# Kernel tuning notes

Hardware: AMD Instinct MI355X
Metric: run time of the kernel (lower is better)

## Reference

```python
import jax, jax.numpy as jnp
import numpy as np

D_MODEL = 512
N_HEADS = 8
KV_OPTS = (8, 4, 1)
D_K = D_MODEL // N_HEADS


def setup_inputs() -> dict:
    key = jax.random.key(0)
    ks = jax.random.split(key, 32)
    it = iter(ks)
    s = 0.02
    inp = {"x": jax.random.normal(next(it), (64, 1024, D_MODEL), dtype=jnp.float32)}
    # router params
    inp["r_w1"] = jax.random.normal(next(it), (D_MODEL, D_MODEL // 4), jnp.float32) * s
    inp["r_b1"] = jnp.zeros((D_MODEL // 4,), jnp.float32)
    inp["r_w2"] = jax.random.normal(next(it), (D_MODEL // 4, len(KV_OPTS)), jnp.float32) * s
    inp["r_b2"] = jnp.zeros((len(KV_OPTS),), jnp.float32)
    # per-expert GQA params
    for i, nkv in enumerate(KV_OPTS):
        inp[f"wq{i}"] = jax.random.normal(next(it), (D_MODEL, D_MODEL), jnp.float32) * s
        inp[f"wk{i}"] = jax.random.normal(next(it), (D_MODEL, nkv * D_K), jnp.float32) * s
        inp[f"wv{i}"] = jax.random.normal(next(it), (D_MODEL, nkv * D_K), jnp.float32) * s
        inp[f"wo{i}"] = jax.random.normal(next(it), (D_MODEL, D_MODEL), jnp.float32) * s
    return inp


def gqa(x, wq, wk, wv, wo, n_kv):
    B, S, _ = x.shape
    groups = N_HEADS // n_kv
    q = (x @ wq).reshape(B, S, N_HEADS, D_K).transpose(0, 2, 1, 3)  # [B,H,S,Dk]
    k = (x @ wk).reshape(B, S, n_kv, D_K).transpose(0, 2, 1, 3)     # [B,Kv,S,Dk]
    v = (x @ wv).reshape(B, S, n_kv, D_K).transpose(0, 2, 1, 3)
    k = jnp.repeat(k, groups, axis=1)
    v = jnp.repeat(v, groups, axis=1)
    scores = jnp.einsum('bhqd,bhkd->bhqk', q, k) / jnp.sqrt(jnp.float32(D_K))
    attn = jax.nn.softmax(scores, axis=-1)
    out = jnp.einsum('bhqk,bhkd->bhqd', attn, v)
    out = out.transpose(0, 2, 1, 3).reshape(B, S, D_MODEL)
    return out @ wo


def reference(x, r_w1, r_b1, r_w2, r_b2,
              wq0, wk0, wv0, wo0,
              wq1, wk1, wv1, wo1,
              wq2, wk2, wv2, wo2):
    routing_input = x.mean(axis=1)                      # [B, D]
    logits = jax.nn.relu(routing_input @ r_w1 + r_b1) @ r_w2 + r_b2
    sel = jnp.argmax(jax.nn.softmax(logits, axis=-1), axis=-1)  # [B]

    params = [(wq0, wk0, wv0, wo0), (wq1, wk1, wv1, wo1), (wq2, wk2, wv2, wo2)]
    out = jnp.zeros_like(x)
    for i, nkv in enumerate(KV_OPTS):
        yi = gqa(x, *params[i], nkv)                    # [B,S,D]
        mask = (sel == i)[:, None, None]
        out = jnp.where(mask, yi, out)
    return out
```

## Files before the change

### kernel.cpp

```cpp
#include <hip/hip_runtime.h>
#include <hip/hip_bf16.h>

typedef __hip_bfloat16 bf16;
typedef __attribute__((ext_vector_type(8))) short short8;
typedef __attribute__((ext_vector_type(4))) float f32x4;
typedef __attribute__((ext_vector_type(16))) float f32x16;

#define MFMA_BF16(a,b,c) __builtin_amdgcn_mfma_f32_16x16x32_bf16(a,b,c,0,0,0)
#define MFMA32(a,b,c)    __builtin_amdgcn_mfma_f32_32x32x16_bf16(a,b,c,0,0,0)

#if __has_builtin(__builtin_amdgcn_exp2f)
#define EXPFN(x) __builtin_amdgcn_exp2f(x)
#define QSCALE 0.1803368801111204f
#else
#define EXPFN(x) __expf(x)
#define QSCALE 0.125f
#endif

__device__ __forceinline__ unsigned short bfbits(float f){
  bf16 h = __float2bfloat16(f);
  return __builtin_bit_cast(unsigned short, h);
}
__device__ __forceinline__ unsigned packbf(float a, float b){
  return (unsigned)bfbits(a) | ((unsigned)bfbits(b) << 16);
}

__device__ __forceinline__ void glds16(const void* g, void* l){
  __builtin_amdgcn_global_load_lds(
      (const __attribute__((address_space(1))) unsigned int*)(size_t)g,
      (__attribute__((address_space(3))) unsigned int*)l, 16, 0, 0);
}

__global__ __launch_bounds__(256) void xconv(const float* __restrict__ x, bf16* __restrict__ xb){
  size_t i = ((size_t)blockIdx.x*256 + threadIdx.x)*8;
  float4 a = *(const float4*)(x+i);
  float4 b = *(const float4*)(x+i+4);
  union { unsigned short u[8]; uint4 v; } p;
  p.u[0]=bfbits(a.x); p.u[1]=bfbits(a.y); p.u[2]=bfbits(a.z); p.u[3]=bfbits(a.w);
  p.u[4]=bfbits(b.x); p.u[5]=bfbits(b.y); p.u[6]=bfbits(b.z); p.u[7]=bfbits(b.w);
  *(uint4*)(xb+i) = p.v;
}

__global__ __launch_bounds__(256)
void wconv(const float* __restrict__ w0, const float* __restrict__ w1, const float* __restrict__ w2,
           int N0, int N1, int N2, bf16* o0, bf16* o1, bf16* o2){
  int e = blockIdx.z;
  const float* W = e==0?w0:(e==1?w1:w2);
  int N = e==0?N0:(e==1?N1:N2);
  bf16* out = e==0?o0:(e==1?o1:o2);
  int n0 = blockIdx.y*64; if (n0 >= N) return;
  int k0 = blockIdx.x*64;
  __shared__ float tile[64][65];
  int t = threadIdx.x;
#pragma unroll
  for (int j=0;j<16;++j){
    int ee = j*256+t; int r = ee>>6, c = ee&63;
    tile[r][c] = W[(size_t)(k0+r)*N + n0+c];
  }
  __syncthreads();
#pragma unroll
  for (int j=0;j<16;++j){
    int ee = j*256+t; int n = ee>>6, kk = ee&63;
    out[(size_t)(n0+n)*512 + k0+kk] = __float2bfloat16(tile[kk][n]);
  }
}

__global__ void mean_part_kernel(const float* __restrict__ x, float* __restrict__ part){
  int b = blockIdx.x, ch = blockIdx.y;
  const float* xb = x + ((size_t)b*1024 + (size_t)ch*64)*512;
  for (int dd = threadIdx.x; dd < 512; dd += 256){
    float a = 0.f;
    for (int s = 0; s < 64; ++s) a += xb[(size_t)s*512 + dd];
    part[((size_t)b*16 + ch)*512 + dd] = a;
  }
}

__global__ void mean_final_kernel(const float* __restrict__ part, float* __restrict__ ri){
  int b = blockIdx.x;
  for (int dd = threadIdx.x; dd < 512; dd += 256){
    float a = 0.f;
    for (int c = 0; c < 16; ++c) a += part[((size_t)b*16 + c)*512 + dd];
    ri[(size_t)b*512 + dd] = a * (1.f/1024.f);
  }
}

__global__ void router_kernel(const float* __restrict__ ri,
                              const float* __restrict__ w1, const float* __restrict__ b1,
                              const float* __restrict__ w2, const float* __restrict__ b2,
                              int* __restrict__ sel){
  int b = blockIdx.x, t = threadIdx.x;
  __shared__ float h[128];
  __shared__ float lg[3];
  const float* rib = ri + (size_t)b*512;
  float acc = b1[t];
  for (int d = 0; d < 512; ++d) acc += rib[d]*w1[(size_t)d*128 + t];
  h[t] = fmaxf(acc, 0.f);
  __syncthreads();
  if (t < 3){
    float a = b2[t];
    for (int j = 0; j < 128; ++j) a += h[j]*w2[j*3 + t];
    lg[t] = a;
  }
  __syncthreads();
  if (t == 0){
    int best = 0; float bv = lg[0];
    if (lg[1] > bv){ bv = lg[1]; best = 1; }
    if (lg[2] > bv){ bv = lg[2]; best = 2; }
    sel[b] = best;
  }
}

template<int OUTMODE>
__global__ __launch_bounds__(256)
void gemm_mfma(const bf16* __restrict__ A,
               const bf16* __restrict__ Wt0, const bf16* __restrict__ Wt1, const bf16* __restrict__ Wt2,
               int N0, int N1, int N2,
               const int* __restrict__ sel, float oscale,
               void* __restrict__ outp){
  int b = blockIdx.z;
  int se = sel[b];
  const bf16* W = se==0?Wt0:(se==1?Wt1:Wt2);
  int N = se==0?N0:(se==1?N1:N2);
  int nb = blockIdx.y*64;
  if (nb >= N) return;
  int mb = blockIdx.x*128;
  __shared__ __align__(16) bf16 As[128*64];
  __shared__ __align__(16) bf16 Bs[64*64];
  int t = threadIdx.x, lane = t&63, w = t>>6, gg = lane>>4, cl = lane&15;
  f32x4 acc[2][4] = {};
  const bf16* Ab = A + ((size_t)b*1024 + mb)*512;
  const bf16* Wb = W + (size_t)nb*512;

  for (int k0 = 0; k0 < 512; k0 += 64){
#pragma unroll
    for (int j=0;j<4;++j){
      int o = (j*256+t)*16;
      int r = o>>7;
      int gs = ((o>>4)&7) ^ (r&7);
      glds16(Ab + (size_t)r*512 + k0 + gs*8, (char*)As + o);
    }
#pragma unroll
    for (int j=0;j<2;++j){
      int o = (j*256+t)*16;
      int r = o>>7;
      int gs = ((o>>4)&7) ^ (r&7);
      glds16(Wb + (size_t)r*512 + k0 + gs*8, (char*)Bs + o);
    }
    __syncthreads();

    short8 af[2][2], bfr[4][2];
#pragma unroll
    for (int mf=0;mf<2;++mf)
#pragma unroll
      for (int ks=0;ks<2;++ks){
        int r = w*32 + mf*16 + cl;
        int off = (ks*64 + gg*16) ^ ((r&7)<<4);
        af[mf][ks] = *(const short8*)((const char*)As + r*128 + off);
      }
#pragma unroll
    for (int nf=0;nf<4;++nf)
#pragma unroll
      for (int ks=0;ks<2;++ks){
        int r = nf*16 + cl;
        int off = (ks*64 + gg*16) ^ ((r&7)<<4);
        bfr[nf][ks] = *(const short8*)((const char*)Bs + r*128 + off);
      }
#pragma unroll
    for (int mf=0;mf<2;++mf)
#pragma unroll
      for (int nf=0;nf<4;++nf)
#pragma unroll
        for (int ks=0;ks<2;++ks)
          acc[mf][nf] = MFMA_BF16(af[mf][ks], bfr[nf][ks], acc[mf][nf]);
    __syncthreads();
  }

#pragma unroll
  for (int mf=0;mf<2;++mf)
#pragma unroll
    for (int nf=0;nf<4;++nf){
      int row = mb + w*32 + mf*16 + gg*4;
      int col = nb + nf*16 + cl;
      if (OUTMODE==0){
        bf16* C = (bf16*)outp;
#pragma unroll
        for (int i=0;i<4;++i)
          C[((size_t)b*1024 + row+i)*512 + col] = __float2bfloat16(acc[mf][nf][i]*oscale);
      } else if (OUTMODE==1){
        union { unsigned short u[4]; uint2 v; } pk;
#pragma unroll
        for (int i=0;i<4;++i) pk.u[i] = bfbits(acc[mf][nf][i]);
        *(uint2*)((bf16*)outp + ((size_t)b*512 + col)*1024 + row) = pk.v;
      } else {
        float* C = (float*)outp;
#pragma unroll
        for (int i=0;i<4;++i)
          C[((size_t)b*1024 + row+i)*512 + col] = acc[mf][nf][i];
      }
    }
}

__global__ __launch_bounds__(256, 4)
void attn_mfma(const bf16* __restrict__ Q, const bf16* __restrict__ K,
               const bf16* __restrict__ Vt, const int* __restrict__ sel,
               bf16* __restrict__ AO){
  int b = blockIdx.z, h = blockIdx.y, q0 = blockIdx.x*128;
  int se = sel[b];
  int nkv = se==0?8:(se==1?4:1);
  int kvh = h/(8/nkv);
  __shared__ __align__(16) bf16 Ks[2][64*64];
  __shared__ __align__(16) bf16 Vs[2][64*64];
  int t = threadIdx.x, l = t&63, w = t>>6, cl = l&31, hi = l>>5;
  const bf16* Kb = K + (size_t)b*1024*512 + (size_t)kvh*64;
  const bf16* Vb = Vt + ((size_t)b*512 + (size_t)kvh*64)*1024;
  const bf16* Qg = Q + ((size_t)b*1024 + q0 + w*32 + cl)*512 + h*64;

  short8 qf0 = *(const short8*)(Qg + hi*8);
  short8 qf1 = *(const short8*)(Qg + 16 + hi*8);
  short8 qf2 = *(const short8*)(Qg + 32 + hi*8);
  short8 qf3 = *(const short8*)(Qg + 48 + hi*8);

  f32x16 accO0 = {}, accO1 = {};
  float lrow = 0.f;
  int swz = (cl&7)<<4;

#define STAGE(CUR, S0) { \
  _Pragma("unroll") for (int j=0;j<2;++j){ \
    int o = (j*256+t)*16; int r = o>>7; int gs = ((o>>4)&7)^(r&7); \
    glds16(Kb + (size_t)((S0)+r)*512 + gs*8, (char*)Ks[CUR] + o); \
    glds16(Vb + (size_t)r*1024 + (S0) + gs*8, (char*)Vs[CUR] + o); \
  } }

  STAGE(0, 0)
  __syncthreads();
  int cur = 0;
  for (int kt=0; kt<16; ++kt){
    if (kt<15) STAGE(cur^1, (kt+1)*64)

    const char* Kt_ = (const char*)Ks[cur];
    const char* Vt_ = (const char*)Vs[cur];

    f32x16 sc0 = {}, sc1 = {};
#pragma unroll
    for (int ks=0;ks<4;++ks){
      int off = (ks*32 + hi*16) ^ swz;
      short8 kf0 = *(const short8*)(Kt_ + (size_t)cl*128 + off);
      short8 kf1 = *(const short8*)(Kt_ + (size_t)(32+cl)*128 + off);
      short8 qq = ks==0?qf0:(ks==1?qf1:(ks==2?qf2:qf3));
      sc0 = MFMA32(kf0, qq, sc0);
      sc1 = MFMA32(kf1, qq, sc1);
    }

    float ts0=0.f, ts1=0.f, ts2=0.f, ts3=0.f;
#pragma unroll
    for (int r=0;r<16;r+=2){
      float a0 = EXPFN(sc0[r]);   float a1 = EXPFN(sc0[r+1]);
      float a2 = EXPFN(sc1[r]);   float a3 = EXPFN(sc1[r+1]);
      sc0[r]=a0; sc0[r+1]=a1; sc1[r]=a2; sc1[r+1]=a3;
      ts0+=a0; ts1+=a1; ts2+=a2; ts3+=a3;
    }
    lrow += (ts0+ts1)+(ts2+ts3);

    unsigned pA0[4],pB0[4],pA1[4],pB1[4];
#pragma unroll
    for (int m=0;m<4;++m){
      pA0[m]=packbf(sc0[4*m+0],sc0[4*m+1]); pB0[m]=packbf(sc0[4*m+2],sc0[4*m+3]);
      pA1[m]=packbf(sc1[4*m+0],sc1[4*m+1]); pB1[m]=packbf(sc1[4*m+2],sc1[4*m+3]);
    }
    unsigned oA0[4],oB0[4],oA1[4],oB1[4];
#pragma unroll
    for (int m=0;m<4;++m){
      oA0[m]=__shfl_xor(pA0[m],32); oB0[m]=__shfl_xor(pB0[m],32);
      oA1[m]=__shfl_xor(pA1[m],32); oB1[m]=__shfl_xor(pB1[m],32);
    }
    short8 pF[4];
#pragma unroll
    for (int f=0;f<2;++f){
      uint4 u;
      u.x = hi ? oA0[2*f+1] : pA0[2*f];
      u.y = hi ? oB0[2*f+1] : pB0[2*f];
      u.z = hi ? pA0[2*f+1] : oA0[2*f];
      u.w = hi ? pB0[2*f+1] : oB0[2*f];
      pF[f] = __builtin_bit_cast(short8, u);
      uint4 v;
      v.x = hi ? oA1[2*f+1] : pA1[2*f];
      v.y = hi ? oB1[2*f+1] : pB1[2*f];
      v.z = hi ? pA1[2*f+1] : oA1[2*f];
      v.w = hi ? pB1[2*f+1] : oB1[2*f];
      pF[2+f] = __builtin_bit_cast(short8, v);
    }

#pragma unroll
    for (int ks2=0;ks2<4;++ks2){
      int off = (ks2*32 + hi*16) ^ swz;
      short8 vf0 = *(const short8*)(Vt_ + (size_t)cl*128 + off);
      short8 vf1 = *(const short8*)(Vt_ + (size_t)(32+cl)*128 + off);
      accO0 = MFMA32(vf0, pF[ks2], accO0);
      accO1 = MFMA32(vf1, pF[ks2], accO1);
    }
    __syncthreads();
    cur ^= 1;
  }
#undef STAGE

  float lfull = lrow + __shfl_xor(lrow, 32);
  float inv = 1.f/lfull;
  int row = q0 + w*32 + cl;
  bf16* Ao = AO + ((size_t)b*1024 + row)*512 + h*64;
#pragma unroll
  for (int u=0;u<4;++u){
    union{ unsigned short s[4]; uint2 v; } P0, P1;
#pragma unroll
    for (int j2=0;j2<4;++j2){
      P0.s[j2] = bfbits(accO0[4*u+j2]*inv);
      P1.s[j2] = bfbits(accO1[4*u+j2]*inv);
    }
    *(uint2*)(Ao + 8*u + 4*hi) = P0.v;
    *(uint2*)(Ao + 32 + 8*u + 4*hi) = P1.v;
  }
}

extern "C" void kernel_launch(void* const* d_in, const int* in_sizes, int n_in,
                              void* d_out, int out_size, void* d_ws, size_t ws_size,
                              hipStream_t stream){
  const float* x    = (const float*)d_in[0];
  const float* r_w1 = (const float*)d_in[1];
  const float* r_b1 = (const float*)d_in[2];
  const float* r_w2 = (const float*)d_in[3];
  const float* r_b2 = (const float*)d_in[4];
  const float* wq[3] = {(const float*)d_in[5], (const float*)d_in[9],  (const float*)d_in[13]};
  const float* wk[3] = {(const float*)d_in[6], (const float*)d_in[10], (const float*)d_in[14]};
  const float* wv[3] = {(const float*)d_in[7], (const float*)d_in[11], (const float*)d_in[15]};
  const float* wo[3] = {(const float*)d_in[8], (const float*)d_in[12], (const float*)d_in[16]};

  char* ws = (char*)d_ws;
  int*   sel      = (int*)ws;
  float* ri       = (float*)(ws + 4096);
  float* partials = (float*)(ws + 4096 + 131072);
  bf16*  Wtbuf    = (bf16*)(ws + 4096 + 131072 + 2097152);
  const size_t NE = (size_t)64*1024*512;
  bf16* xb = (bf16*)(ws + ((size_t)4<<20));
  bf16* Qb = xb + NE;
  bf16* Kb = Qb + NE;
  bf16* Vt = Kb + NE;
  bf16* AO = xb;

  xconv<<<16384, 256, 0, stream>>>(x, xb);
  mean_part_kernel<<<dim3(64,16), 256, 0, stream>>>(x, partials);
  mean_final_kernel<<<64, 256, 0, stream>>>(partials, ri);
  router_kernel<<<64, 128, 0, stream>>>(ri, r_w1, r_b1, r_w2, r_b2, sel);

  {
    bf16 *o0 = Wtbuf, *o1 = o0 + (size_t)512*512, *o2 = o1 + (size_t)512*512;
    wconv<<<dim3(8,8,3), 256, 0, stream>>>(wq[0],wq[1],wq[2], 512,512,512, o0,o1,o2);
    gemm_mfma<0><<<dim3(8,8,64), 256, 0, stream>>>(xb, o0,o1,o2, 512,512,512, sel, (float)QSCALE, Qb);
  }
  {
    bf16 *o0 = Wtbuf, *o1 = o0 + (size_t)512*512, *o2 = o1 + (size_t)256*512;
    wconv<<<dim3(8,8,3), 256, 0, stream>>>(wk[0],wk[1],wk[2], 512,256,64, o0,o1,o2);
    gemm_mfma<0><<<dim3(8,8,64), 256, 0, stream>>>(xb, o0,o1,o2, 512,256,64, sel, 1.0f, Kb);
  }
  {
    bf16 *o0 = Wtbuf, *o1 = o0 + (size_t)512*512, *o2 = o1 + (size_t)256*512;
    wconv<<<dim3(8,8,3), 256, 0, stream>>>(wv[0],wv[1],wv[2], 512,256,64, o0,o1,o2);
    gemm_mfma<1><<<dim3(8,8,64), 256, 0, stream>>>(xb, o0,o1,o2, 512,256,64, sel, 1.0f, Vt);
  }

  attn_mfma<<<dim3(8,8,64), 256, 0, stream>>>(Qb, Kb, Vt, sel, AO);

  {
    bf16 *o0 = Wtbuf, *o1 = o0 + (size_t)512*512, *o2 = o1 + (size_t)512*512;
    wconv<<<dim3(8,8,3), 256, 0, stream>>>(wo[0],wo[1],wo[2], 512,512,512, o0,o1,o2);
    gemm_mfma<2><<<dim3(8,8,64), 256, 0, stream>>>(AO, o0,o1,o2, 512,512,512, sel, 1.0f, (float*)d_out);
  }
}
```

Before: 466.7 us.

## Fuse x conversion with mean partials, widen GEMM N tile, tweak attention scheduling

Merges the fp32-to-bf16 conversion of x with the per-chunk mean partial sums, so x is read once instead of twice. Templates the projection GEMM on its N tile width and uses 128-wide tiles for the Q and output projections, giving more A-tile reuse per block and fewer blocks. In attention, raises wave priority around the MFMA loops and halves the cross-lane shuffles when building the P fragments. The wider tile raises register and LDS use per block, and the fused conversion kernel runs fewer, longer blocks.

Measured after the change: 441.2 us. 5.5% less time.

```diff
diff --git a/kernel.cpp b/kernel.cpp
--- a/kernel.cpp
+++ b/kernel.cpp
@@ -31,14 +31,31 @@
       (__attribute__((address_space(3))) unsigned int*)l, 16, 0, 0);
 }
 
-__global__ __launch_bounds__(256) void xconv(const float* __restrict__ x, bf16* __restrict__ xb){
-  size_t i = ((size_t)blockIdx.x*256 + threadIdx.x)*8;
-  float4 a = *(const float4*)(x+i);
-  float4 b = *(const float4*)(x+i+4);
-  union { unsigned short u[8]; uint4 v; } p;
-  p.u[0]=bfbits(a.x); p.u[1]=bfbits(a.y); p.u[2]=bfbits(a.z); p.u[3]=bfbits(a.w);
-  p.u[4]=bfbits(b.x); p.u[5]=bfbits(b.y); p.u[6]=bfbits(b.z); p.u[7]=bfbits(b.w);
-  *(uint4*)(xb+i) = p.v;
+__global__ __launch_bounds__(256)
+void xconv_mean(const float* __restrict__ x, bf16* __restrict__ xb, float* __restrict__ part){
+  int b = blockIdx.x, ch = blockIdx.y, t = threadIdx.x;
+  size_t base = ((size_t)b*1024 + (size_t)ch*64)*512;
+  const float2* xp = (const float2*)(x + base);
+  unsigned* op = (unsigned*)(xb + base);
+  float s0 = 0.f, s1 = 0.f;
+#pragma unroll 4
+  for (int s = 0; s < 64; ++s){
+    float2 v = xp[s*256 + t];
+    s0 += v.x; s1 += v.y;
+    op[s*256 + t] = packbf(v.x, v.y);
+  }
+  float* pp = part + ((size_t)b*16 + ch)*512;
+  pp[2*t]   = s0;
+  pp[2*t+1] = s1;
+}
+
+__global__ void mean_final_kernel(const float* __restrict__ part, float* __restrict__ ri){
+  int b = blockIdx.x;
+  for (int dd = threadIdx.x; dd < 512; dd += 256){
+    float a = 0.f;
+    for (int c = 0; c < 16; ++c) a += part[((size_t)b*16 + c)*512 + dd];
+    ri[(size_t)b*512 + dd] = a * (1.f/1024.f);
+  }
 }
 
 __global__ __launch_bounds__(256)
@@ -62,25 +79,6 @@
   for (int j=0;j<16;++j){
     int ee = j*256+t; int n = ee>>6, kk = ee&63;
     out[(size_t)(n0+n)*512 + k0+kk] = __float2bfloat16(tile[kk][n]);
-  }
-}
-
-__global__ void mean_part_kernel(const float* __restrict__ x, float* __restrict__ part){
-  int b = blockIdx.x, ch = blockIdx.y;
-  const float* xb = x + ((size_t)b*1024 + (size_t)ch*64)*512;
-  for (int dd = threadIdx.x; dd < 512; dd += 256){
-    float a = 0.f;
-    for (int s = 0; s < 64; ++s) a += xb[(size_t)s*512 + dd];
-    part[((size_t)b*16 + ch)*512 + dd] = a;
-  }
-}
-
-__global__ void mean_final_kernel(const float* __restrict__ part, float* __restrict__ ri){
-  int b = blockIdx.x;
-  for (int dd = threadIdx.x; dd < 512; dd += 256){
-    float a = 0.f;
-    for (int c = 0; c < 16; ++c) a += part[((size_t)b*16 + c)*512 + dd];
-    ri[(size_t)b*512 + dd] = a * (1.f/1024.f);
   }
 }
 
@@ -110,7 +108,7 @@
   }
 }
 
-template<int OUTMODE>
+template<int OUTMODE, int BN>
 __global__ __launch_bounds__(256)
 void gemm_mfma(const bf16* __restrict__ A,
                const bf16* __restrict__ Wt0, const bf16* __restrict__ Wt1, const bf16* __restrict__ Wt2,
@@ -121,13 +119,13 @@
   int se = sel[b];
   const bf16* W = se==0?Wt0:(se==1?Wt1:Wt2);
   int N = se==0?N0:(se==1?N1:N2);
-  int nb = blockIdx.y*64;
+  int nb = blockIdx.y*BN;
   if (nb >= N) return;
   int mb = blockIdx.x*128;
   __shared__ __align__(16) bf16 As[128*64];
-  __shared__ __align__(16) bf16 Bs[64*64];
+  __shared__ __align__(16) bf16 Bs[BN*64];
   int t = threadIdx.x, lane = t&63, w = t>>6, gg = lane>>4, cl = lane&15;
-  f32x4 acc[2][4] = {};
+  f32x4 acc[2][BN/16] = {};
   const bf16* Ab = A + ((size_t)b*1024 + mb)*512;
   const bf16* Wb = W + (size_t)nb*512;
 
@@ -140,7 +138,7 @@
       glds16(Ab + (size_t)r*512 + k0 + gs*8, (char*)As + o);
     }
 #pragma unroll
-    for (int j=0;j<2;++j){
+    for (int j=0;j<BN/32;++j){
       int o = (j*256+t)*16;
       int r = o>>7;
       int gs = ((o>>4)&7) ^ (r&7);
@@ -148,7 +146,7 @@
     }
     __syncthreads();
 
-    short8 af[2][2], bfr[4][2];
+    short8 af[2][2];
 #pragma unroll
     for (int mf=0;mf<2;++mf)
 #pragma unroll
@@ -158,27 +156,23 @@
         af[mf][ks] = *(const short8*)((const char*)As + r*128 + off);
       }
 #pragma unroll
-    for (int nf=0;nf<4;++nf)
-#pragma unroll
-      for (int ks=0;ks<2;++ks){
-        int r = nf*16 + cl;
-        int off = (ks*64 + gg*16) ^ ((r&7)<<4);
-        bfr[nf][ks] = *(const short8*)((const char*)Bs + r*128 + off);
-      }
-#pragma unroll
-    for (int mf=0;mf<2;++mf)
-#pragma unroll
-      for (int nf=0;nf<4;++nf)
-#pragma unroll
-        for (int ks=0;ks<2;++ks)
-          acc[mf][nf] = MFMA_BF16(af[mf][ks], bfr[nf][ks], acc[mf][nf]);
+    for (int nf=0;nf<BN/16;++nf){
+      int r = nf*16 + cl;
+      int rs = (r&7)<<4;
+      short8 b0 = *(const short8*)((const char*)Bs + r*128 + ((0*64 + gg*16) ^ rs));
+      short8 b1 = *(const short8*)((const char*)Bs + r*128 + ((1*64 + gg*16) ^ rs));
+      acc[0][nf] = MFMA_BF16(af[0][0], b0, acc[0][nf]);
+      acc[0][nf] = MFMA_BF16(af[0][1], b1, acc[0][nf]);
+      acc[1][nf] = MFMA_BF16(af[1][0], b0, acc[1][nf]);
+      acc[1][nf] = MFMA_BF16(af[1][1], b1, acc[1][nf]);
+    }
     __syncthreads();
   }
 
 #pragma unroll
   for (int mf=0;mf<2;++mf)
 #pragma unroll
-    for (int nf=0;nf<4;++nf){
+    for (int nf=0;nf<BN/16;++nf){
       int row = mb + w*32 + mf*16 + gg*4;
       int col = nb + nf*16 + cl;
       if (OUTMODE==0){
@@ -241,6 +235,7 @@
     const char* Vt_ = (const char*)Vs[cur];
 
     f32x16 sc0 = {}, sc1 = {};
+    __builtin_amdgcn_s_setprio(1);
 #pragma unroll
     for (int ks=0;ks<4;++ks){
       int off = (ks*32 + hi*16) ^ swz;
@@ -250,6 +245,7 @@
       sc0 = MFMA32(kf0, qq, sc0);
       sc1 = MFMA32(kf1, qq, sc1);
     }
+    __builtin_amdgcn_s_setprio(0);
 
     float ts0=0.f, ts1=0.f, ts2=0.f, ts3=0.f;
 #pragma unroll
@@ -267,29 +263,32 @@
       pA0[m]=packbf(sc0[4*m+0],sc0[4*m+1]); pB0[m]=packbf(sc0[4*m+2],sc0[4*m+3]);
       pA1[m]=packbf(sc1[4*m+0],sc1[4*m+1]); pB1[m]=packbf(sc1[4*m+2],sc1[4*m+3]);
     }
-    unsigned oA0[4],oB0[4],oA1[4],oB1[4];
-#pragma unroll
-    for (int m=0;m<4;++m){
-      oA0[m]=__shfl_xor(pA0[m],32); oB0[m]=__shfl_xor(pB0[m],32);
-      oA1[m]=__shfl_xor(pA1[m],32); oB1[m]=__shfl_xor(pB1[m],32);
+    unsigned rA0[2],rB0[2],rA1[2],rB1[2];
+#pragma unroll
+    for (int f=0;f<2;++f){
+      rA0[f] = __shfl_xor(hi ? pA0[2*f] : pA0[2*f+1], 32);
+      rB0[f] = __shfl_xor(hi ? pB0[2*f] : pB0[2*f+1], 32);
+      rA1[f] = __shfl_xor(hi ? pA1[2*f] : pA1[2*f+1], 32);
+      rB1[f] = __shfl_xor(hi ? pB1[2*f] : pB1[2*f+1], 32);
     }
     short8 pF[4];
 #pragma unroll
     for (int f=0;f<2;++f){
       uint4 u;
-      u.x = hi ? oA0[2*f+1] : pA0[2*f];
-      u.y = hi ? oB0[2*f+1] : pB0[2*f];
-      u.z = hi ? pA0[2*f+1] : oA0[2*f];
-      u.w = hi ? pB0[2*f+1] : oB0[2*f];
+      u.x = hi ? rA0[f]     : pA0[2*f];
+      u.y = hi ? rB0[f]     : pB0[2*f];
+      u.z = hi ? pA0[2*f+1] : rA0[f];
+      u.w = hi ? pB0[2*f+1] : rB0[f];
       pF[f] = __builtin_bit_cast(short8, u);
       uint4 v;
-      v.x = hi ? oA1[2*f+1] : pA1[2*f];
-      v.y = hi ? oB1[2*f+1] : pB1[2*f];
-      v.z = hi ? pA1[2*f+1] : oA1[2*f];
-      v.w = hi ? pB1[2*f+1] : oB1[2*f];
+      v.x = hi ? rA1[f]     : pA1[2*f];
+      v.y = hi ? rB1[f]     : pB1[2*f];
+      v.z = hi ? pA1[2*f+1] : rA1[f];
+      v.w = hi ? pB1[2*f+1] : rB1[f];
       pF[2+f] = __builtin_bit_cast(short8, v);
     }
 
+    __builtin_amdgcn_s_setprio(1);
 #pragma unroll
     for (int ks2=0;ks2<4;++ks2){
       int off = (ks2*32 + hi*16) ^ swz;
@@ -298,6 +297,7 @@
       accO0 = MFMA32(vf0, pF[ks2], accO0);
       accO1 = MFMA32(vf1, pF[ks2], accO1);
     }
+    __builtin_amdgcn_s_setprio(0);
     __syncthreads();
     cur ^= 1;
   }
@@ -345,25 +345,24 @@
   bf16* Vt = Kb + NE;
   bf16* AO = xb;
 
-  xconv<<<16384, 256, 0, stream>>>(x, xb);
-  mean_part_kernel<<<dim3(64,16), 256, 0, stream>>>(x, partials);
+  xconv_mean<<<dim3(64,16), 256, 0, stream>>>(x, xb, partials);
   mean_final_kernel<<<64, 256, 0, stream>>>(partials, ri);
   router_kernel<<<64, 128, 0, stream>>>(ri, r_w1, r_b1, r_w2, r_b2, sel);
 
   {
     bf16 *o0 = Wtbuf, *o1 = o0 + (size_t)512*512, *o2 = o1 + (size_t)512*512;
     wconv<<<dim3(8,8,3), 256, 0, stream>>>(wq[0],wq[1],wq[2], 512,512,512, o0,o1,o2);
-    gemm_mfma<0><<<dim3(8,8,64), 256, 0, stream>>>(xb, o0,o1,o2, 512,512,512, sel, (float)QSCALE, Qb);
+    gemm_mfma<0,128><<<dim3(8,4,64), 256, 0, stream>>>(xb, o0,o1,o2, 512,512,512, sel, (float)QSCALE, Qb);
   }
   {
     bf16 *o0 = Wtbuf, *o1 = o0 + (size_t)512*512, *o2 = o1 + (size_t)256*512;
     wconv<<<dim3(8,8,3), 256, 0, stream>>>(wk[0],wk[1],wk[2], 512,256,64, o0,o1,o2);
-    gemm_mfma<0><<<dim3(8,8,64), 256, 0, stream>>>(xb, o0,o1,o2, 512,256,64, sel, 1.0f, Kb);
+    gemm_mfma<0,64><<<dim3(8,8,64), 256, 0, stream>>>(xb, o0,o1,o2, 512,256,64, sel, 1.0f, Kb);
   }
   {
     bf16 *o0 = Wtbuf, *o1 = o0 + (size_t)512*512, *o2 = o1 + (size_t)256*512;
     wconv<<<dim3(8,8,3), 256, 0, stream>>>(wv[0],wv[1],wv[2], 512,256,64, o0,o1,o2);
-    gemm_mfma<1><<<dim3(8,8,64), 256, 0, stream>>>(xb, o0,o1,o2, 512,256,64, sel, 1.0f, Vt);
+    gemm_mfma<1,64><<<dim3(8,8,64), 256, 0, stream>>>(xb, o0,o1,o2, 512,256,64, sel, 1.0f, Vt);
   }
 
   attn_mfma<<<dim3(8,8,64), 256, 0, stream>>>(Qb, Kb, Vt, sel, AO);
@@ -371,6 +370,6 @@
   {
     bf16 *o0 = Wtbuf, *o1 = o0 + (size_t)512*512, *o2 = o1 + (size_t)512*512;
     wconv<<<dim3(8,8,3), 256, 0, stream>>>(wo[0],wo[1],wo[2], 512,512,512, o0,o1,o2);
-    gemm_mfma<2><<<dim3(8,8,64), 256, 0, stream>>>(AO, o0,o1,o2, 512,512,512, sel, 1.0f, (float*)d_out);
-  }
-}
+    gemm_mfma<2,128><<<dim3(8,4,64), 256, 0, stream>>>(AO, o0,o1,o2, 512,512,512, sel, 1.0f, (float*)d_out);
+  }
+}
```
